# Kernel optimization log

Measured on AMD Instinct MI355X. Metric: run time of the kernel, lower is better.

## Reference

```python
import jax, jax.numpy as jnp
import numpy as np

HIDDEN = 512
HEADS = 8
HEAD_DIM = HIDDEN // HEADS


def setup_inputs() -> dict:
    key = jax.random.key(0)
    ks = jax.random.split(key, 12)
    B, S = 2, 2048
    s = 1.0 / np.sqrt(HIDDEN)
    inp = {
        "query": jax.random.normal(ks[0], (B, S, HIDDEN), dtype=jnp.float32),
        "key": jax.random.normal(ks[1], (B, S, HIDDEN), dtype=jnp.float32),
        "value": jax.random.normal(ks[2], (B, S, HIDDEN), dtype=jnp.float32),
        "Wq": jax.random.uniform(ks[3], (HIDDEN, HIDDEN), jnp.float32, -s, s),
        "bq": jnp.zeros((HIDDEN,), jnp.float32),
        "Wk": jax.random.uniform(ks[4], (HIDDEN, HIDDEN), jnp.float32, -s, s),
        "bk": jnp.zeros((HIDDEN,), jnp.float32),
        "Wv": jax.random.uniform(ks[5], (HIDDEN, HIDDEN), jnp.float32, -s, s),
        "bv": jnp.zeros((HIDDEN,), jnp.float32),
        "Wo": jax.random.uniform(ks[6], (HIDDEN, HIDDEN), jnp.float32, -s, s),
        "bo": jnp.zeros((HIDDEN,), jnp.float32),
    }
    return inp


def reference(query, key, value, Wq, bq, Wk, bk, Wv, bv, Wo, bo):
    B, S, _ = query.shape
    scale = jnp.sqrt(jnp.asarray(HEAD_DIM, dtype=query.dtype))
    # Linear projections (torch Linear: x @ W.T + b)
    Q = (query @ Wq.T + bq).reshape(B, S, HEADS, HEAD_DIM).transpose(0, 2, 1, 3)
    K = (key @ Wk.T + bk).reshape(B, S, HEADS, HEAD_DIM).transpose(0, 2, 1, 3)
    V = (value @ Wv.T + bv).reshape(B, S, HEADS, HEAD_DIM).transpose(0, 2, 1, 3)
    # Scores: [B, H, S, S]
    energy = jnp.einsum("bhqd,bhkd->bhqk", Q, K) / scale
    attn = jax.nn.softmax(energy, axis=-1)
    # Dropout is identity in eval mode.
    x = jnp.einsum("bhqk,bhkd->bhqd", attn, V)
    x = x.transpose(0, 2, 1, 3).reshape(B, S, HIDDEN)
    return x @ Wo.T + bo
```

## Files before the change

kernel.cpp:

```cpp
#include <hip/hip_runtime.h>

typedef __bf16 bf16x8 __attribute__((ext_vector_type(8)));
typedef float f32x4 __attribute__((ext_vector_type(4)));
typedef unsigned int uint4v __attribute__((ext_vector_type(4)));
typedef unsigned int uint2v __attribute__((ext_vector_type(2)));

__device__ __forceinline__ unsigned short f2bf(float f) {
  union { float f; unsigned int u; } v; v.f = f;
  unsigned int u = v.u;
  u += 0x7FFFu + ((u >> 16) & 1u);
  return (unsigned short)(u >> 16);
}

__device__ __forceinline__ unsigned int pack2bf(float a, float b) {
  return (unsigned int)f2bf(a) | ((unsigned int)f2bf(b) << 16);
}

__global__ __launch_bounds__(256) void convert_w(
    const float* wq, const float* wk, const float* wv, const float* wo,
    unsigned short* wqc, unsigned short* wkc, unsigned short* wvc,
    unsigned short* woc, float qscale)
{
  const float* src; unsigned short* dst; float sc = 1.f;
  switch (blockIdx.y) {
    case 0: src = wq; dst = wqc; sc = qscale; break;
    case 1: src = wk; dst = wkc; break;
    case 2: src = wv; dst = wvc; break;
    default: src = wo; dst = woc; break;
  }
  int idx = (blockIdx.x * 256 + threadIdx.x) * 8;
  f32x4 a = *(const f32x4*)(src + idx);
  f32x4 b = *(const f32x4*)(src + idx + 4);
  uint4v p;
  p.x = pack2bf(a.x * sc, a.y * sc);
  p.y = pack2bf(a.z * sc, a.w * sc);
  p.z = pack2bf(b.x * sc, b.y * sc);
  p.w = pack2bf(b.z * sc, b.w * sc);
  *(uint4v*)(dst + idx) = p;
}

template<int OUT, bool AF32>
__device__ __forceinline__ void gemm_core(
    const void* __restrict__ Ap, const unsigned short* __restrict__ W,
    const float* __restrict__ bias, void* __restrict__ Cp,
    float bscale, int mbase, int nbase)
{
  __shared__ union {
    struct { unsigned short As[64][40]; unsigned short Bs[128][40]; } t;
    unsigned short Cs[128][72];
  } u;

  const int tid  = threadIdx.x;
  const int wave = tid >> 6, lane = tid & 63;
  const int lrow = lane & 15, lgrp = lane >> 4;
  const int ar = tid >> 2, ac = (tid & 3) * 8;

  const unsigned short* Bg0 = W + (size_t)(nbase + ar) * 512 + ac;
  const unsigned short* Bg1 = W + (size_t)(nbase + ar + 64) * 512 + ac;

  f32x4 acc[4][2];
#pragma unroll
  for (int i = 0; i < 4; i++)
#pragma unroll
    for (int j = 0; j < 2; j++) acc[i][j] = (f32x4){0.f, 0.f, 0.f, 0.f};

  const unsigned short* Ab = (const unsigned short*)Ap;
  const float*          Af = (const float*)Ap;
  uint4v pA; f32x4 pAf0, pAf1;
  if constexpr (AF32) {
    const float* base = Af + (size_t)(mbase + ar) * 512 + ac;
    pAf0 = *(const f32x4*)(base);
    pAf1 = *(const f32x4*)(base + 4);
  } else {
    pA = *(const uint4v*)(Ab + (size_t)(mbase + ar) * 512 + ac);
  }
  uint4v pB0 = *(const uint4v*)Bg0;
  uint4v pB1 = *(const uint4v*)Bg1;

  for (int kt = 0; kt < 512; kt += 32) {
    __syncthreads();
    if constexpr (AF32) {
      uint4v w;
      w.x = pack2bf(pAf0.x, pAf0.y); w.y = pack2bf(pAf0.z, pAf0.w);
      w.z = pack2bf(pAf1.x, pAf1.y); w.w = pack2bf(pAf1.z, pAf1.w);
      *(uint4v*)&u.t.As[ar][ac] = w;
    } else {
      *(uint4v*)&u.t.As[ar][ac] = pA;
    }
    *(uint4v*)&u.t.Bs[ar][ac]      = pB0;
    *(uint4v*)&u.t.Bs[ar + 64][ac] = pB1;
    __syncthreads();
    if (kt + 32 < 512) {
      if constexpr (AF32) {
        const float* base = Af + (size_t)(mbase + ar) * 512 + ac + kt + 32;
        pAf0 = *(const f32x4*)(base);
        pAf1 = *(const f32x4*)(base + 4);
      } else {
        pA = *(const uint4v*)(Ab + (size_t)(mbase + ar) * 512 + ac + kt + 32);
      }
      pB0 = *(const uint4v*)(Bg0 + kt + 32);
      pB1 = *(const uint4v*)(Bg1 + kt + 32);
    }
    bf16x8 a[4], b[2];
#pragma unroll
    for (int mi = 0; mi < 4; mi++)
      a[mi] = *(const bf16x8*)&u.t.As[mi * 16 + lrow][lgrp * 8];
#pragma unroll
    for (int ni = 0; ni < 2; ni++)
      b[ni] = *(const bf16x8*)&u.t.Bs[wave * 32 + ni * 16 + lrow][lgrp * 8];
#pragma unroll
    for (int mi = 0; mi < 4; mi++)
#pragma unroll
      for (int ni = 0; ni < 2; ni++)
        acc[mi][ni] = __builtin_amdgcn_mfma_f32_16x16x32_bf16(
            a[mi], b[ni], acc[mi][ni], 0, 0, 0);
  }

  if constexpr (OUT == 2) {
    __syncthreads();
#pragma unroll
    for (int ni = 0; ni < 2; ni++) {
      int col_l = wave * 32 + ni * 16 + lrow;
      float bv = bias[nbase + col_l];
#pragma unroll
      for (int mi = 0; mi < 4; mi++) {
        int row_l = mi * 16 + lgrp * 4;
#pragma unroll
        for (int r = 0; r < 4; r++)
          u.Cs[col_l][row_l + r] = f2bf(acc[mi][ni][r] + bv);
      }
    }
    __syncthreads();
    const int bb = mbase >> 11, s_base = mbase & 2047;
    unsigned short* Vt = (unsigned short*)Cp;
#pragma unroll
    for (int ks = 0; ks < 4; ks++) {
      int seg = tid + ks * 256;
      int c = seg >> 3, r0 = (seg & 7) * 8;
      uint4v val = *(const uint4v*)&u.Cs[c][r0];
      int n = nbase + c, hh = n >> 6, d = n & 63;
      *(uint4v*)(Vt + ((size_t)(bb * 8 + hh) * 64 + d) * 2048 + s_base + r0) = val;
    }
  } else {
#pragma unroll
    for (int ni = 0; ni < 2; ni++) {
      int col = nbase + wave * 32 + ni * 16 + lrow;
      float bv = bias[col] * bscale;
#pragma unroll
      for (int mi = 0; mi < 4; mi++) {
        int row0 = mbase + mi * 16 + lgrp * 4;
#pragma unroll
        for (int r = 0; r < 4; r++) {
          float val = acc[mi][ni][r] + bv;
          if constexpr (OUT == 0)
            ((unsigned short*)Cp)[(size_t)(row0 + r) * 512 + col] = f2bf(val);
          else
            ((float*)Cp)[(size_t)(row0 + r) * 512 + col] = val;
        }
      }
    }
  }
}

__global__ __launch_bounds__(256) void qkv_gemm(
    const float* q, const float* k, const float* v,
    const unsigned short* wqc, const unsigned short* wkc,
    const unsigned short* wvc,
    const float* bq, const float* bk, const float* bv,
    unsigned short* Qb, unsigned short* Kb, unsigned short* Vt, float qscale)
{
  const int z = blockIdx.z;
  const int mb = blockIdx.y * 64, nb = blockIdx.x * 128;
  if (z == 2)      gemm_core<2, true>(v, wvc, bv, Vt, 1.f, mb, nb);
  else if (z == 0) gemm_core<0, true>(q, wqc, bq, Qb, qscale, mb, nb);
  else             gemm_core<0, true>(k, wkc, bk, Kb, 1.f, mb, nb);
}

__global__ __launch_bounds__(256) void out_gemm(
    const unsigned short* ctx, const unsigned short* woc,
    const float* bo, float* out)
{
  gemm_core<1, false>(ctx, woc, bo, out, 1.f, blockIdx.y * 64, blockIdx.x * 128);
}

__global__ __launch_bounds__(256) void attn_kernel(
    const unsigned short* Qb, const unsigned short* Kb,
    const unsigned short* Vt, unsigned short* ctx)
{
  __shared__ unsigned short Ks[128][74];
  __shared__ unsigned short Vs[64][140];
  __shared__ unsigned short Ps[2][64][76];

  const int tid  = threadIdx.x;
  const int wave = tid >> 6, lane = tid & 63;
  const int lrow = lane & 15, lgrp = lane >> 4;
  const int qh = wave >> 1, kh = wave & 1;
  const int bh = blockIdx.y, b = bh >> 3, h = bh & 7;
  const int qbase = blockIdx.x * 64;

  const unsigned short* Qg  = Qb + (size_t)(b * 2048 + qbase) * 512 + h * 64;
  const unsigned short* Kg  = Kb + (size_t)(b * 2048) * 512 + h * 64;
  const unsigned short* Vtg = Vt + (size_t)bh * 64 * 2048;

#pragma unroll
  for (int i = 0; i < 2; i++) {
    int seg = tid + i * 256;
    int row = seg >> 3, c0 = (seg & 7) * 8;
    *(uint4v*)&Ps[0][row][c0] = *(const uint4v*)(Qg + (size_t)row * 512 + c0);
  }
  __syncthreads();
  bf16x8 qf[2][2];
#pragma unroll
  for (int mi = 0; mi < 2; mi++)
#pragma unroll
    for (int c = 0; c < 2; c++)
      qf[mi][c] = *(const bf16x8*)&Ps[0][qh * 32 + mi * 16 + lrow][c * 32 + lgrp * 8];

  const int s0 = tid >> 3, kc_ = (tid & 7) * 8;
  const int krow0 = ((s0 & 15) << 3) | (s0 >> 4);
  const int vd_ = tid >> 4, vcl = (tid & 15);

  float lst[2][4] = {{0.f,0.f,0.f,0.f},{0.f,0.f,0.f,0.f}};
  f32x4 oacc[2][4];
#pragma unroll
  for (int mi = 0; mi < 2; mi++)
#pragma unroll
    for (int d = 0; d < 4; d++) oacc[mi][d] = (f32x4){0.f, 0.f, 0.f, 0.f};

  uint4v kr[4], vr[4];
#pragma unroll
  for (int i = 0; i < 4; i++) {
    kr[i] = *(const uint4v*)(Kg + (size_t)(krow0 + 2 * i) * 512 + kc_);
    vr[i] = *(const uint4v*)(Vtg + (size_t)(vd_ + 16 * i) * 2048 + vcl * 8);
  }

  for (int it = 0; it < 16; ++it) {
    __syncthreads();
#pragma unroll
    for (int i = 0; i < 4; i++) {
      *(uint4v*)&Ks[s0 + 32 * i][kc_] = kr[i];
      *(uint2v*)&Vs[vd_ + 16 * i][vcl * 4]      = (uint2v){vr[i].x, vr[i].y};
      *(uint2v*)&Vs[vd_ + 16 * i][64 + vcl * 4] = (uint2v){vr[i].z, vr[i].w};
    }
    __syncthreads();
    if (it < 15) {
      const int key0 = (it + 1) * 128;
#pragma unroll
      for (int i = 0; i < 4; i++) {
        kr[i] = *(const uint4v*)(Kg + (size_t)(key0 + krow0 + 2 * i) * 512 + kc_);
        vr[i] = *(const uint4v*)(Vtg + (size_t)(vd_ + 16 * i) * 2048 + key0 + vcl * 8);
      }
    }

    f32x4 sacc[2][4];
#pragma unroll
    for (int mi = 0; mi < 2; mi++)
#pragma unroll
      for (int ni = 0; ni < 4; ni++) sacc[mi][ni] = (f32x4){0.f, 0.f, 0.f, 0.f};
#pragma unroll
    for (int ni = 0; ni < 4; ni++) {
      const int t = 4 * kh + ni;
      bf16x8 k0 = *(const bf16x8*)&Ks[t * 16 + lrow][lgrp * 8];
      bf16x8 k1 = *(const bf16x8*)&Ks[t * 16 + lrow][32 + lgrp * 8];
#pragma unroll
      for (int mi = 0; mi < 2; mi++) {
        sacc[mi][ni] = __builtin_amdgcn_mfma_f32_16x16x32_bf16(qf[mi][0], k0, sacc[mi][ni], 0, 0, 0);
        sacc[mi][ni] = __builtin_amdgcn_mfma_f32_16x16x32_bf16(qf[mi][1], k1, sacc[mi][ni], 0, 0, 0);
      }
    }

#pragma unroll
    for (int mi = 0; mi < 2; mi++)
#pragma unroll
      for (int ni = 0; ni < 4; ni++)
#pragma unroll
        for (int r = 0; r < 4; r++) {
          float p = exp2f(sacc[mi][ni][r]);
          sacc[mi][ni][r] = p;
          lst[mi][r] += p;
        }

#pragma unroll
    for (int mi = 0; mi < 2; mi++)
#pragma unroll
      for (int r = 0; r < 4; r++) {
        uint2v pk;
        pk.x = pack2bf(sacc[mi][0][r], sacc[mi][1][r]);
        pk.y = pack2bf(sacc[mi][2][r], sacc[mi][3][r]);
        *(uint2v*)&Ps[kh][qh * 32 + mi * 16 + lgrp * 4 + r][lrow * 4] = pk;
      }

#pragma unroll
    for (int ks = 0; ks < 2; ks++) {
      bf16x8 pa[2];
#pragma unroll
      for (int mi = 0; mi < 2; mi++)
        pa[mi] = *(const bf16x8*)&Ps[kh][qh * 32 + mi * 16 + lrow][ks * 32 + lgrp * 8];
#pragma unroll
      for (int dt = 0; dt < 4; dt++) {
        bf16x8 vb = *(const bf16x8*)&Vs[dt * 16 + lrow][kh * 64 + ks * 32 + lgrp * 8];
#pragma unroll
        for (int mi = 0; mi < 2; mi++)
          oacc[mi][dt] = __builtin_amdgcn_mfma_f32_16x16x32_bf16(pa[mi], vb, oacc[mi][dt], 0, 0, 0);
      }
    }
  }

#pragma unroll
  for (int m = 1; m < 16; m <<= 1)
#pragma unroll
    for (int mi = 0; mi < 2; mi++)
#pragma unroll
      for (int r = 0; r < 4; r++) lst[mi][r] += __shfl_xor(lst[mi][r], m, 64);

  __syncthreads();
  float* Obuf = (float*)&Ks[0][0];
  float* Lbuf = (float*)&Vs[0][0];
  if (kh == 1) {
#pragma unroll
    for (int mi = 0; mi < 2; mi++)
#pragma unroll
      for (int r = 0; r < 4; r++) {
        int row = qh * 32 + mi * 16 + lgrp * 4 + r;
#pragma unroll
        for (int dt = 0; dt < 4; dt++)
          Obuf[row * 68 + dt * 16 + lrow] = oacc[mi][dt][r];
        if (lrow == 0) Lbuf[row] = lst[mi][r];
      }
  }
  __syncthreads();
  if (kh == 0) {
    unsigned short* Cg = ctx + (size_t)(b * 2048 + qbase) * 512 + h * 64;
#pragma unroll
    for (int mi = 0; mi < 2; mi++)
#pragma unroll
      for (int r = 0; r < 4; r++) {
        int row = qh * 32 + mi * 16 + lgrp * 4 + r;
        float inv = 1.0f / (lst[mi][r] + Lbuf[row]);
#pragma unroll
        for (int dt = 0; dt < 4; dt++) {
          float val = (oacc[mi][dt][r] + Obuf[row * 68 + dt * 16 + lrow]) * inv;
          Cg[(size_t)(qbase >= 0 ? row : row) * 512 + dt * 16 + lrow] = f2bf(val);
        }
      }
  }
}

extern "C" void kernel_launch(void* const* d_in, const int* in_sizes, int n_in,
                              void* d_out, int out_size, void* d_ws, size_t ws_size,
                              hipStream_t stream)
{
  const float* q  = (const float*)d_in[0];
  const float* k  = (const float*)d_in[1];
  const float* v  = (const float*)d_in[2];
  const float* Wq = (const float*)d_in[3];
  const float* bq = (const float*)d_in[4];
  const float* Wk = (const float*)d_in[5];
  const float* bk = (const float*)d_in[6];
  const float* Wv = (const float*)d_in[7];
  const float* bv = (const float*)d_in[8];
  const float* Wo = (const float*)d_in[9];
  const float* bo = (const float*)d_in[10];
  float* out = (float*)d_out;

  unsigned short* wqc = (unsigned short*)d_ws;
  unsigned short* wkc = wqc + (1 << 18);
  unsigned short* wvc = wkc + (1 << 18);
  unsigned short* woc = wvc + (1 << 18);
  unsigned short* Qb  = woc + (1 << 18);
  unsigned short* Kb  = Qb  + (1 << 21);
  unsigned short* Vt  = Kb  + (1 << 21);
  unsigned short* Cb  = Vt  + (1 << 21);

  const float qscale = 0.125f * 1.44269504088896340736f;

  convert_w<<<dim3(128, 4), 256, 0, stream>>>(
      Wq, Wk, Wv, Wo, wqc, wkc, wvc, woc, qscale);
  qkv_gemm<<<dim3(4, 64, 3), 256, 0, stream>>>(
      q, k, v, wqc, wkc, wvc, bq, bk, bv, Qb, Kb, Vt, qscale);
  attn_kernel<<<dim3(32, 16), 256, 0, stream>>>(Qb, Kb, Vt, Cb);
  out_gemm<<<dim3(4, 64), 256, 0, stream>>>(Cb, woc, bo, out);
}
```

Measured before the change: 159.8 us.

## Compute softmax row sums via MFMA against a ones tile; truncate P to bf16

Appends a ones-filled row tile to the V shared buffer so an extra MFMA column block accumulates the softmax denominators, replacing the per-element scalar adds and the cross-lane shuffle reduction. The exp uses the raw hardware exp2 builtin, and P is packed to bf16 by truncation with a byte permute instead of round-to-nearest. This cuts VALU work in the softmax stage at the cost of extra MFMAs, more LDS and more accumulator registers, and it slightly changes numerics (the sum now uses the bf16-rounded P, and truncation adds bias).

```diff
diff --git a/kernel.cpp b/kernel.cpp
--- a/kernel.cpp
+++ b/kernel.cpp
@@ -14,6 +14,11 @@
 
 __device__ __forceinline__ unsigned int pack2bf(float a, float b) {
   return (unsigned int)f2bf(a) | ((unsigned int)f2bf(b) << 16);
+}
+
+__device__ __forceinline__ unsigned int packtrunc(float a, float b) {
+  return __builtin_amdgcn_perm(__float_as_uint(b), __float_as_uint(a),
+                               0x07060302u);
 }
 
 __global__ __launch_bounds__(256) void convert_w(
@@ -188,7 +193,7 @@
     const unsigned short* Vt, unsigned short* ctx)
 {
   __shared__ unsigned short Ks[128][74];
-  __shared__ unsigned short Vs[64][140];
+  __shared__ unsigned short Vs[80][140];
   __shared__ unsigned short Ps[2][64][76];
 
   const int tid  = threadIdx.x;
@@ -208,6 +213,11 @@
     int row = seg >> 3, c0 = (seg & 7) * 8;
     *(uint4v*)&Ps[0][row][c0] = *(const uint4v*)(Qg + (size_t)row * 512 + c0);
   }
+  {
+    int row = 64 + (tid >> 4), c0 = (tid & 15) * 8;
+    unsigned int one2 = 0x3F803F80u;
+    *(uint4v*)&Vs[row][c0] = (uint4v){one2, one2, one2, one2};
+  }
   __syncthreads();
   bf16x8 qf[2][2];
 #pragma unroll
@@ -220,12 +230,11 @@
   const int krow0 = ((s0 & 15) << 3) | (s0 >> 4);
   const int vd_ = tid >> 4, vcl = (tid & 15);
 
-  float lst[2][4] = {{0.f,0.f,0.f,0.f},{0.f,0.f,0.f,0.f}};
-  f32x4 oacc[2][4];
+  f32x4 oacc[2][5];
 #pragma unroll
   for (int mi = 0; mi < 2; mi++)
 #pragma unroll
-    for (int d = 0; d < 4; d++) oacc[mi][d] = (f32x4){0.f, 0.f, 0.f, 0.f};
+    for (int d = 0; d < 5; d++) oacc[mi][d] = (f32x4){0.f, 0.f, 0.f, 0.f};
 
   uint4v kr[4], vr[4];
 #pragma unroll
@@ -274,19 +283,15 @@
 #pragma unroll
       for (int ni = 0; ni < 4; ni++)
 #pragma unroll
-        for (int r = 0; r < 4; r++) {
-          float p = exp2f(sacc[mi][ni][r]);
-          sacc[mi][ni][r] = p;
-          lst[mi][r] += p;
-        }
-
+        for (int r = 0; r < 4; r++)
+          sacc[mi][ni][r] = __builtin_amdgcn_exp2f(sacc[mi][ni][r]);
 #pragma unroll
     for (int mi = 0; mi < 2; mi++)
 #pragma unroll
       for (int r = 0; r < 4; r++) {
         uint2v pk;
-        pk.x = pack2bf(sacc[mi][0][r], sacc[mi][1][r]);
-        pk.y = pack2bf(sacc[mi][2][r], sacc[mi][3][r]);
+        pk.x = packtrunc(sacc[mi][0][r], sacc[mi][1][r]);
+        pk.y = packtrunc(sacc[mi][2][r], sacc[mi][3][r]);
         *(uint2v*)&Ps[kh][qh * 32 + mi * 16 + lgrp * 4 + r][lrow * 4] = pk;
       }
 
@@ -297,7 +302,7 @@
       for (int mi = 0; mi < 2; mi++)
         pa[mi] = *(const bf16x8*)&Ps[kh][qh * 32 + mi * 16 + lrow][ks * 32 + lgrp * 8];
 #pragma unroll
-      for (int dt = 0; dt < 4; dt++) {
+      for (int dt = 0; dt < 5; dt++) {
         bf16x8 vb = *(const bf16x8*)&Vs[dt * 16 + lrow][kh * 64 + ks * 32 + lgrp * 8];
 #pragma unroll
         for (int mi = 0; mi < 2; mi++)
@@ -305,13 +310,6 @@
       }
     }
   }
-
-#pragma unroll
-  for (int m = 1; m < 16; m <<= 1)
-#pragma unroll
-    for (int mi = 0; mi < 2; mi++)
-#pragma unroll
-      for (int r = 0; r < 4; r++) lst[mi][r] += __shfl_xor(lst[mi][r], m, 64);
 
   __syncthreads();
   float* Obuf = (float*)&Ks[0][0];
@@ -325,7 +323,7 @@
 #pragma unroll
         for (int dt = 0; dt < 4; dt++)
           Obuf[row * 68 + dt * 16 + lrow] = oacc[mi][dt][r];
-        if (lrow == 0) Lbuf[row] = lst[mi][r];
+        if (lrow == 0) Lbuf[row] = oacc[mi][4][r];
       }
   }
   __syncthreads();
@@ -336,11 +334,11 @@
 #pragma unroll
       for (int r = 0; r < 4; r++) {
         int row = qh * 32 + mi * 16 + lgrp * 4 + r;
-        float inv = 1.0f / (lst[mi][r] + Lbuf[row]);
+        float inv = 1.0f / (oacc[mi][4][r] + Lbuf[row]);
 #pragma unroll
         for (int dt = 0; dt < 4; dt++) {
           float val = (oacc[mi][dt][r] + Obuf[row * 68 + dt * 16 + lrow]) * inv;
-          Cg[(size_t)(qbase >= 0 ? row : row) * 512 + dt * 16 + lrow] = f2bf(val);
+          Cg[(size_t)row * 512 + dt * 16 + lrow] = f2bf(val);
         }
       }
   }
```

Result: faster. 150.4 us (-5.8%).
